# Kernel optimization log

Measured on AMD Instinct MI355X. Metric: run time of the kernel, lower is better.

## Reference

```python
import jax, jax.numpy as jnp
import numpy as np

B, N, L = 256, 4096, 6
EMBED, HID, VOCAB = 16, 32, 200
NOTE, LSTM_D, T = 64, 64, 128


def _tree_structure():
    """One random tree of N nodes (root=node 0), tiled across the batch.
    height = distance above deepest descendant; children have strictly smaller height."""
    rng = np.random.default_rng(0)
    height = np.zeros(N, np.int32)
    height[0] = L
    height[1:] = rng.integers(0, L, N - 1)
    kind = np.full(N, 2, np.int32)  # 2 = internal
    leaf_mask = height == 0
    kind[leaf_mask] = (rng.random(leaf_mask.sum()) < 0.1).astype(np.int32)  # 1=ptr, 0=leaf
    parent = np.zeros(N, np.int64)
    for hl in range(L):
        mask = height == hl
        cand = np.where((height > hl) & (kind == 2))[0]  # root always qualifies
        parent[mask] = rng.choice(cand, size=int(mask.sum()))
    parent[0] = 0  # root points to itself; harmless (its own h stays 0 until final level)
    return height, kind, parent


def setup_inputs():
    height, kind, parent = _tree_structure()
    offs = (np.arange(B, dtype=np.int64) * N)[:, None]
    rng = np.random.default_rng(1)
    inp = {
        'kind': jnp.asarray(np.tile(kind, B), jnp.int32),
        'height': jnp.asarray(np.tile(height, B), jnp.int32),
        'parent': jnp.asarray((parent[None, :] + offs).reshape(-1), jnp.int32),
        'tok_a': jnp.asarray(rng.integers(0, VOCAB, B * N), jnp.int32),
        'tok_b': jnp.asarray(rng.integers(0, VOCAB, B * N), jnp.int32),
        'ptr_time': jnp.asarray(rng.integers(0, T, B * N), jnp.int32),
    }
    key = jax.random.key(0)
    ks = jax.random.split(key, 16)
    def w(k, shape, scale=0.05):
        return (jax.random.normal(k, shape, jnp.float32) * scale)
    inp['first_notes'] = w(ks[0], (B, NOTE), 1.0)
    inp['lstm_out'] = w(ks[1], (B, T, LSTM_D), 1.0)
    inp['embedding'] = w(ks[2], (VOCAB, EMBED), 0.02)
    inp['leaf_w1'] = w(ks[3], (2 * EMBED, HID)); inp['leaf_b1'] = w(ks[4], (HID,))
    inp['leaf_w2'] = w(ks[5], (HID, HID));       inp['leaf_b2'] = w(ks[6], (HID,))
    inp['node_w'] = w(ks[7], (2 * EMBED + HID, HID)); inp['node_b'] = w(ks[8], (HID,))
    inp['ptr_w'] = w(ks[9], (NOTE + LSTM_D, HID));    inp['ptr_b'] = w(ks[10], (HID,))
    inp['ff_w1'] = w(ks[11], (HID, HID)); inp['ff_b1'] = w(ks[12], (HID,))
    inp['ff_w2'] = w(ks[13], (HID, HID)); inp['ff_b2'] = w(ks[14], (HID,))
    inp['tail_w'] = w(ks[15], (HID, 1)); inp['tail_b'] = jnp.zeros((1,), jnp.float32)
    return inp


def reference(kind, height, parent, tok_a, tok_b, ptr_time, first_notes, lstm_out,
              embedding, leaf_w1, leaf_b1, leaf_w2, leaf_b2, node_w, node_b,
              ptr_w, ptr_b, ff_w1, ff_b1, ff_w2, ff_b2, tail_w, tail_b):
    M = kind.shape[0]
    nb = first_notes.shape[0]
    n_per = M // nb
    tree_id = jnp.arange(M, dtype=jnp.int32) // n_per
    emb_a = embedding[tok_a]  # [M, EMBED] (parent-type / first-token embed)
    emb_b = embedding[tok_b]  # [M, EMBED] (node-type / second-token embed)
    pair = jnp.concatenate([emb_a, emb_b], axis=-1)  # [M, 2*EMBED]
    # leaf path: two stacked linears (no nonlinearity), as in leaf_ff
    leaf_h = (pair @ leaf_w1 + leaf_b1) @ leaf_w2 + leaf_b2
    # ptr path: Linear(note_dim + lstm_out_dim -> hidden)
    ptr_in = jnp.concatenate([first_notes[tree_id], lstm_out[tree_id, ptr_time]], axis=-1)
    ptr_h = ptr_in @ ptr_w + ptr_b
    h = jnp.where((kind == 0)[:, None], leaf_h,
                  jnp.where((kind == 1)[:, None], ptr_h, 0.0))
    # level-synchronous child-sum: children always have smaller height
    for lvl in range(1, L + 1):
        csum = jax.ops.segment_sum(h, parent, num_segments=M)  # [M, HID]
        inner = jax.nn.relu(jnp.concatenate([pair, csum], axis=-1) @ node_w + node_b)
        h = jnp.where((height == lvl)[:, None], inner, h)
    roots = h[::n_per]  # [B, HID], root is node 0 of each tree block
    ff = (roots @ ff_w1 + ff_b1) @ ff_w2 + ff_b2
    return ff @ tail_w + tail_b  # [B, 1]


if __name__ == '__main__':
    out = reference(**setup_inputs())
    print(out.shape, out.dtype)
```

## Files before the change

### kernel.cpp

```cpp
#include <hip/hip_runtime.h>

#define BATCH   256
#define N_PER   4096
#define EMBED   16
#define HID     32
#define NOTE    64
#define LSTM_D  64
#define T_LEN   128
#define VOCAB   200
#define HSTR    (BATCH * HID)

#define MH_C0    0
#define MH_C1    1
#define MH_CNT   2
#define MH_P     7
#define MH_PBASE 8
#define OFF_K0N   64
#define OFF_K0S   (OFF_K0N + N_PER)
#define OFF_K1N   (OFF_K0S + N_PER)
#define OFF_K1S   (OFF_K1N + N_PER)
#define OFF_PLIST (OFF_K1S + N_PER)
#define OFF_WSLOT (OFF_PLIST + N_PER)
#define OFF_COFF  (OFF_WSLOT + N_PER)
#define EAW_OFF     (1024 * 1024)
#define EBW_OFF     (EAW_OFF + VOCAB * HID * 4)
#define LA2_OFF     (EBW_OFF + VOCAB * HID * 4)
#define LB2_OFF     (LA2_OFF + VOCAB * HID * 4)
#define CC_OFF      (LB2_OFF + VOCAB * HID * 4)
#define H_OFF       (8ull * 1024 * 1024)

__device__ __forceinline__ unsigned long long shflup64(unsigned long long x, int off) {
    unsigned lo = (unsigned)(x & 0xffffffffull);
    unsigned hi = (unsigned)(x >> 32);
    lo = __shfl_up(lo, off, 64);
    hi = __shfl_up(hi, off, 64);
    return ((unsigned long long)hi << 32) | (unsigned long long)lo;
}

__global__ __launch_bounds__(1024) void build_structure(
    const int* __restrict__ kind, const int* __restrict__ height,
    const int* __restrict__ parent, int* __restrict__ meta,
    const float* __restrict__ embedding,
    const float* __restrict__ leaf_w1, const float* __restrict__ leaf_b1,
    const float* __restrict__ leaf_w2, const float* __restrict__ leaf_b2,
    const float* __restrict__ node_w,
    float* __restrict__ eaw_g, float* __restrict__ ebw_g,
    float* __restrict__ la2, float* __restrict__ lb2, float* __restrict__ cc)
{
    __shared__ unsigned long long wlo[16], whi[16];
    __shared__ int wint[16];
    __shared__ int node2pidx[N_PER];
    __shared__ int deg[N_PER];
    __shared__ int sbases[8];
    __shared__ int stot[8];

    int t  = threadIdx.x;
    int i0 = 4 * t;
    int laneid = t & 63;
    int wid    = t >> 6;

    int par[4], hgt4[4], kn4[4];
    #pragma unroll
    for (int q = 0; q < 4; ++q) {
        par[q]  = parent[i0 + q];
        hgt4[q] = height[i0 + q];
        kn4[q]  = kind[i0 + q];
    }

    int myb[4];
    #pragma unroll
    for (int q = 0; q < 4; ++q) {
        int hgt = hgt4[q];
        int b;
        if (hgt > 0) { b = 1 + hgt; if (b > 7) b = 7; }
        else b = (kn4[q] == 0) ? 0 : 1;
        myb[q] = b;
    }
    unsigned long long clo = 0, chi = 0;
    #pragma unroll
    for (int q = 0; q < 4; ++q) {
        int b = myb[q];
        if (b < 4) clo += 1ull << (16 * b);
        else       chi += 1ull << (16 * (b - 4));
    }

    unsigned long long a = clo, b64 = chi;
    #pragma unroll
    for (int off = 1; off < 64; off <<= 1) {
        unsigned long long ua = shflup64(a, off);
        unsigned long long ub = shflup64(b64, off);
        if (laneid >= off) { a += ua; b64 += ub; }
    }
    if (laneid == 63) { wlo[wid] = a; whi[wid] = b64; }
    __syncthreads();
    unsigned long long blo = 0, bhi = 0;
    for (int w = 0; w < wid; ++w) { blo += wlo[w]; bhi += whi[w]; }
    unsigned long long inc_lo = a + blo, inc_hi = b64 + bhi;
    if (t == 0) {
        unsigned long long tlo = 0, thi = 0;
        for (int w = 0; w < 16; ++w) { tlo += wlo[w]; thi += whi[w]; }
        stot[0] = (int)(tlo & 0xFFFF);         stot[1] = (int)((tlo >> 16) & 0xFFFF);
        stot[2] = (int)((tlo >> 32) & 0xFFFF); stot[3] = (int)((tlo >> 48) & 0xFFFF);
        stot[4] = (int)(thi & 0xFFFF);         stot[5] = (int)((thi >> 16) & 0xFFFF);
        stot[6] = (int)((thi >> 32) & 0xFFFF); stot[7] = (int)((thi >> 48) & 0xFFFF);
        int s = 0;
        for (int bb = 0; bb < 8; ++bb) { sbases[bb] = s; s += stot[bb]; }
        meta[MH_C0] = stot[0];
        meta[MH_C1] = stot[1];
        for (int l = 0; l < 5; ++l) meta[MH_CNT + l]   = stot[2 + l];
        for (int l = 0; l < 5; ++l) meta[MH_PBASE + l] = sbases[2 + l] - sbases[2];
        meta[MH_P] = (sbases[7] - sbases[2]) + stot[7];
    }
    __syncthreads();

    unsigned long long exlo = inc_lo - clo, exhi = inc_hi - chi;
    int mypos[4], mypidx[4];
    #pragma unroll
    for (int q = 0; q < 4; ++q) {
        int i = i0 + q, b = myb[q];
        int pos;
        if (b < 4) { pos = (int)((exlo >> (16 * b)) & 0xFFFF); exlo += 1ull << (16 * b); }
        else       { pos = (int)((exhi >> (16 * (b - 4))) & 0xFFFF); exhi += 1ull << (16 * (b - 4)); }
        mypos[q] = pos;
        int pidx = -1;
        if (b == 0)      meta[OFF_K0N + pos] = i;
        else if (b == 1) meta[OFF_K1N + pos] = i;
        else {
            pidx = (sbases[b] - sbases[2]) + pos;
            meta[OFF_PLIST + pidx] = i;
            node2pidx[i] = pidx;
        }
        mypidx[q] = pidx;
    }
    #pragma unroll
    for (int q = 0; q < 4; ++q) deg[i0 + q] = 0;
    __syncthreads();

    #pragma unroll
    for (int q = 0; q < 4; ++q) {
        int i = i0 + q;
        if (i != 0) atomicAdd(&deg[node2pidx[par[q]]], 1);
    }
    __syncthreads();

    int d0 = deg[i0], d1 = deg[i0 + 1], d2 = deg[i0 + 2], d3 = deg[i0 + 3];
    int s4 = d0 + d1 + d2 + d3;

    int vi = s4;
    #pragma unroll
    for (int off = 1; off < 64; off <<= 1) {
        int u = __shfl_up(vi, off, 64);
        if (laneid >= off) vi += u;
    }
    if (laneid == 63) wint[wid] = vi;
    __syncthreads();
    int bint = 0;
    for (int w = 0; w < wid; ++w) bint += wint[w];
    int incl = vi + bint;

    int ex = incl - s4;
    int o0 = ex, o1 = ex + d0, o2 = o1 + d1, o3 = o2 + d2;
    deg[i0] = o0; deg[i0 + 1] = o1; deg[i0 + 2] = o2; deg[i0 + 3] = o3;
    meta[OFF_COFF + i0]     = o0;
    meta[OFF_COFF + i0 + 1] = o1;
    meta[OFF_COFF + i0 + 2] = o2;
    meta[OFF_COFF + i0 + 3] = o3;
    if (t == 1023) meta[OFF_COFF + N_PER] = o3 + d3;
    __syncthreads();

    #pragma unroll
    for (int q = 0; q < 4; ++q) {
        int i = i0 + q; if (i == 0) continue;
        int slot = atomicAdd(&deg[node2pidx[par[q]]], 1);
        int b = myb[q];
        if (b == 0)      meta[OFF_K0S + mypos[q]] = slot;
        else if (b == 1) meta[OFF_K1S + mypos[q]] = slot;
        else             meta[OFF_WSLOT + mypidx[q]] = slot;
    }

    {
        int hw = t >> 5, ln = t & 31;
        for (int v = hw; v < VOCAB; v += 32) {
            const float* ev = embedding + v * EMBED;
            float ea = 0.f, eb = 0.f, t1a = 0.f, t1b = 0.f;
            #pragma unroll
            for (int k = 0; k < EMBED; ++k) {
                float e = ev[k];
                ea  += e * node_w[k * HID + ln];
                eb  += e * node_w[(EMBED + k) * HID + ln];
                t1a += e * leaf_w1[k * HID + ln];
                t1b += e * leaf_w1[(EMBED + k) * HID + ln];
            }
            eaw_g[v * HID + ln] = ea;
            ebw_g[v * HID + ln] = eb;
            float a2 = 0.f, b2v = 0.f;
            #pragma unroll
            for (int k = 0; k < HID; ++k) {
                float w2 = leaf_w2[k * HID + ln];
                a2  += __shfl(t1a, k, 32) * w2;
                b2v += __shfl(t1b, k, 32) * w2;
            }
            la2[v * HID + ln] = a2;
            lb2[v * HID + ln] = b2v;
        }
        if (t < HID) {
            float c = leaf_b2[t];
            #pragma unroll
            for (int k = 0; k < HID; ++k) c += leaf_b1[k] * leaf_w2[k * HID + t];
            cc[t] = c;
        }
    }
}

__global__ __launch_bounds__(256) void leaf_kernel(
    const int* __restrict__ meta,
    const int* __restrict__ tok_a, const int* __restrict__ tok_b,
    const float* __restrict__ la2, const float* __restrict__ lb2,
    const float* __restrict__ cc,
    float* __restrict__ h)
{
    int lane = threadIdx.x & 31;
    int gid  = (blockIdx.x * blockDim.x + threadIdx.x) >> 5;
    int ngr  = (gridDim.x * blockDim.x) >> 5;

    float ccv = cc[lane];
    int c0 = meta[MH_C0];
    const int* K0N = meta + OFF_K0N;
    const int* K0S = meta + OFF_K0S;
    int tot = c0 * BATCH;

    for (int base = gid * 8; base < tot; base += ngr * 8) {
        int j = base >> 8, tree0 = base & 255;
        int nd = K0N[j], slot = K0S[j];
        int gnb = tree0 * N_PER + nd;
        int ta[8], tb[8];
        #pragma unroll
        for (int q = 0; q < 8; ++q) {
            ta[q] = tok_a[gnb + q * N_PER];
            tb[q] = tok_b[gnb + q * N_PER];
        }
        float* ob = h + (size_t)slot * HSTR + (size_t)tree0 * HID + lane;
        #pragma unroll
        for (int q = 0; q < 8; ++q)
            ob[q * HID] = ccv + la2[ta[q] * HID + lane] + lb2[tb[q] * HID + lane];
    }
}

__global__ __launch_bounds__(256) void ptr_kernel(
    const int* __restrict__ meta, const int* __restrict__ ptr_time,
    const float* __restrict__ first_notes, const float* __restrict__ lstm_out,
    const float* __restrict__ ptr_w, const float* __restrict__ ptr_b,
    float* __restrict__ h)
{
    __shared__ float pw[(NOTE + LSTM_D) * HID];
    for (int x = threadIdx.x; x < (NOTE + LSTM_D) * HID; x += 256)
        pw[x] = ptr_w[x];
    __syncthreads();

    int lane = threadIdx.x & 31;
    int gid  = (blockIdx.x * blockDim.x + threadIdx.x) >> 5;
    int ngr  = (gridDim.x * blockDim.x) >> 5;

    float pb = ptr_b[lane];
    int c1 = meta[MH_C1];
    const int* K1N = meta + OFF_K1N;
    const int* K1S = meta + OFF_K1S;
    int tot = c1 * BATCH;

    for (int i = gid; i < tot; i += ngr) {
        int j = i >> 8, tree = i & 255;
        int node = K1N[j], slot = K1S[j];
        int gn = tree * N_PER + node;
        int tt = ptr_time[gn];
        const float* fn = first_notes + (size_t)tree * NOTE;
        const float* lo = lstm_out + ((size_t)tree * T_LEN + tt) * LSTM_D;
        float v = pb;
        #pragma unroll
        for (int k = 0; k < NOTE; ++k)   v += fn[k] * pw[k * HID + lane];
        #pragma unroll
        for (int k = 0; k < LSTM_D; ++k) v += lo[k] * pw[(NOTE + k) * HID + lane];
        h[(size_t)slot * HSTR + tree * HID + lane] = v;
    }
}

__global__ __launch_bounds__(256) void level_kernel(
    const int* __restrict__ meta,
    const int* __restrict__ tok_a, const int* __restrict__ tok_b,
    const float* __restrict__ eaw_g, const float* __restrict__ ebw_g,
    const float* __restrict__ node_w, const float* __restrict__ node_b,
    float* __restrict__ h, int lvl)
{
    __shared__ float wlds[HID * HID];
    for (int x = threadIdx.x; x < HID * HID; x += 256)
        wlds[x] = node_w[2 * EMBED * HID + x];
    __syncthreads();

    int cnt = meta[MH_CNT + lvl];
    if (cnt == 0) return;
    int pb  = meta[MH_PBASE + lvl];
    const int* PL = meta + OFF_PLIST;
    const int* WS = meta + OFF_WSLOT;
    const int* CO = meta + OFF_COFF;

    int lane = threadIdx.x & 31;
    int gid  = (blockIdx.x * blockDim.x + threadIdx.x) >> 5;
    int ngr  = (gridDim.x * blockDim.x) >> 5;

    float nb = node_b[lane];
    int perchunk = cnt << 5;
    int tot = cnt * BATCH;

    for (int base = gid * 8; base < tot; base += ngr * 8) {
        int tchunk = base / perchunk;
        int r      = base - tchunk * perchunk;
        int tree0  = (tchunk << 5) + (r & 31);
        int pidx   = pb + (r >> 5);

        int node = PL[pidx], wslot = WS[pidx];
        int e0 = CO[pidx], e1 = CO[pidx + 1];

        int gnb = tree0 * N_PER + node;
        int ta[8], tb[8];
        #pragma unroll
        for (int q = 0; q < 8; ++q) {
            ta[q] = tok_a[gnb + q * N_PER];
            tb[q] = tok_b[gnb + q * N_PER];
        }

        float cs[8] = {0.f,0.f,0.f,0.f,0.f,0.f,0.f,0.f};
        const float* hb = h + (size_t)tree0 * HID + lane;
        for (int c = e0; c < e1; ++c) {
            const float* p = hb + (size_t)c * HSTR;
            #pragma unroll
            for (int q = 0; q < 8; ++q) cs[q] += p[q * HID];
        }

        float v[8];
        #pragma unroll
        for (int q = 0; q < 8; ++q)
            v[q] = nb + eaw_g[ta[q] * HID + lane] + ebw_g[tb[q] * HID + lane];

        #pragma unroll
        for (int k = 0; k < HID; ++k) {
            float w = wlds[k * HID + lane];
            #pragma unroll
            for (int q = 0; q < 8; ++q)
                v[q] += __shfl(cs[q], k, 32) * w;
        }

        float* ob = h + (size_t)wslot * HSTR + (size_t)tree0 * HID + lane;
        #pragma unroll
        for (int q = 0; q < 8; ++q)
            ob[q * HID] = fmaxf(v[q], 0.f);
    }
}

__global__ __launch_bounds__(512) void root_final_kernel(
    const int* __restrict__ meta,
    const int* __restrict__ tok_a, const int* __restrict__ tok_b,
    const float* __restrict__ eaw_g, const float* __restrict__ ebw_g,
    const float* __restrict__ h,
    const float* __restrict__ node_w, const float* __restrict__ node_b,
    const float* __restrict__ ff_w1, const float* __restrict__ ff_b1,
    const float* __restrict__ ff_w2, const float* __restrict__ ff_b2,
    const float* __restrict__ tail_w, const float* __restrict__ tail_b,
    float* __restrict__ out)
{
    __shared__ float part[16][33];
    int tree = blockIdx.x;
    int lane = threadIdx.x & 31;
    int g    = threadIdx.x >> 5;

    const int* CO = meta + OFF_COFF;
    int P = meta[MH_P];
    int e = CO[P - 1], e1 = CO[P];

    const float* hb = h + (size_t)tree * HID + lane;
    float s = 0.f;
    for (int c = e + g; c < e1; c += 16)
        s += hb[(size_t)c * HSTR];
    part[g][lane] = s;
    __syncthreads();

    if (g == 0) {
        float csum = part[0][lane];
        #pragma unroll
        for (int k = 1; k < 16; ++k) csum += part[k][lane];

        int gn = tree * N_PER;
        int ta = tok_a[gn], tb = tok_b[gn];
        float v = node_b[lane] + eaw_g[ta * HID + lane] + ebw_g[tb * HID + lane];
        #pragma unroll
        for (int k = 0; k < HID; ++k)
            v += __shfl(csum, k, 32) * node_w[(2 * EMBED + k) * HID + lane];
        v = fmaxf(v, 0.f);

        float f1 = ff_b1[lane];
        #pragma unroll
        for (int k = 0; k < HID; ++k) f1 += __shfl(v, k, 32) * ff_w1[k * HID + lane];
        float f2 = ff_b2[lane];
        #pragma unroll
        for (int k = 0; k < HID; ++k) f2 += __shfl(f1, k, 32) * ff_w2[k * HID + lane];

        float c2 = f2 * tail_w[lane];
        #pragma unroll
        for (int off = 16; off > 0; off >>= 1) c2 += __shfl_down(c2, off, 32);
        if (lane == 0) out[tree] = c2 + tail_b[0];
    }
}

extern "C" void kernel_launch(void* const* d_in, const int* in_sizes, int n_in,
                              void* d_out, int out_size, void* d_ws, size_t ws_size,
                              hipStream_t stream) {
    const int*   kind        = (const int*)d_in[0];
    const int*   height      = (const int*)d_in[1];
    const int*   parent      = (const int*)d_in[2];
    const int*   tok_a       = (const int*)d_in[3];
    const int*   tok_b       = (const int*)d_in[4];
    const int*   ptr_time    = (const int*)d_in[5];
    const float* first_notes = (const float*)d_in[6];
    const float* lstm_out    = (const float*)d_in[7];
    const float* embedding   = (const float*)d_in[8];
    const float* leaf_w1     = (const float*)d_in[9];
    const float* leaf_b1     = (const float*)d_in[10];
    const float* leaf_w2     = (const float*)d_in[11];
    const float* leaf_b2     = (const float*)d_in[12];
    const float* node_w      = (const float*)d_in[13];
    const float* node_b      = (const float*)d_in[14];
    const float* ptr_w       = (const float*)d_in[15];
    const float* ptr_b       = (const float*)d_in[16];
    const float* ff_w1       = (const float*)d_in[17];
    const float* ff_b1       = (const float*)d_in[18];
    const float* ff_w2       = (const float*)d_in[19];
    const float* ff_b2       = (const float*)d_in[20];
    const float* tail_w      = (const float*)d_in[21];
    const float* tail_b      = (const float*)d_in[22];

    char* ws = (char*)d_ws;
    int*   meta    = (int*)ws;
    float* eaw_g   = (float*)(ws + EAW_OFF);
    float* ebw_g   = (float*)(ws + EBW_OFF);
    float* la2     = (float*)(ws + LA2_OFF);
    float* lb2     = (float*)(ws + LB2_OFF);
    float* cc      = (float*)(ws + CC_OFF);
    float* h       = (float*)(ws + H_OFF);

    build_structure<<<1, 1024, 0, stream>>>(
        kind, height, parent, meta,
        embedding, leaf_w1, leaf_b1, leaf_w2, leaf_b2, node_w,
        eaw_g, ebw_g, la2, lb2, cc);

    leaf_kernel<<<2048, 256, 0, stream>>>(
        meta, tok_a, tok_b, la2, lb2, cc, h);

    ptr_kernel<<<1024, 256, 0, stream>>>(
        meta, ptr_time, first_notes, lstm_out, ptr_w, ptr_b, h);

    for (int lvl = 0; lvl < 5; ++lvl) {
        level_kernel<<<1024, 256, 0, stream>>>(
            meta, tok_a, tok_b, eaw_g, ebw_g, node_w, node_b, h, lvl);
    }

    root_final_kernel<<<BATCH, 512, 0, stream>>>(
        meta, tok_a, tok_b, eaw_g, ebw_g, h, node_w, node_b,
        ff_w1, ff_b1, ff_w2, ff_b2, tail_w, tail_b, (float*)d_out);
}
```

Measured before the change: 407.8 us.

## Fuse leaf, ptr, level and root kernels into one per-tree persistent kernel

Replaces the leaf, pointer, five per-level, and root/final kernels with a single kernel that has one 1024-thread block per tree. Levels are separated by block-level __syncthreads instead of kernel launches. This removes eight launches and the device-wide barriers between them, and keeps ptr_w, node_w and first_notes in LDS per block. In exchange, parallelism drops to 256 blocks, the 8-tree batching per wavefront for coalescing and ILP is lost, and each wavefront now handles one tree, so h accesses become strided.

```diff
diff --git a/kernel.cpp b/kernel.cpp
--- a/kernel.cpp
+++ b/kernel.cpp
@@ -212,200 +212,136 @@
     }
 }
 
-__global__ __launch_bounds__(256) void leaf_kernel(
+__global__ __launch_bounds__(1024) void tree_kernel(
     const int* __restrict__ meta,
     const int* __restrict__ tok_a, const int* __restrict__ tok_b,
+    const int* __restrict__ ptr_time,
+    const float* __restrict__ first_notes, const float* __restrict__ lstm_out,
     const float* __restrict__ la2, const float* __restrict__ lb2,
     const float* __restrict__ cc,
-    float* __restrict__ h)
-{
-    int lane = threadIdx.x & 31;
-    int gid  = (blockIdx.x * blockDim.x + threadIdx.x) >> 5;
-    int ngr  = (gridDim.x * blockDim.x) >> 5;
-
-    float ccv = cc[lane];
-    int c0 = meta[MH_C0];
-    const int* K0N = meta + OFF_K0N;
-    const int* K0S = meta + OFF_K0S;
-    int tot = c0 * BATCH;
-
-    for (int base = gid * 8; base < tot; base += ngr * 8) {
-        int j = base >> 8, tree0 = base & 255;
-        int nd = K0N[j], slot = K0S[j];
-        int gnb = tree0 * N_PER + nd;
-        int ta[8], tb[8];
-        #pragma unroll
-        for (int q = 0; q < 8; ++q) {
-            ta[q] = tok_a[gnb + q * N_PER];
-            tb[q] = tok_b[gnb + q * N_PER];
-        }
-        float* ob = h + (size_t)slot * HSTR + (size_t)tree0 * HID + lane;
-        #pragma unroll
-        for (int q = 0; q < 8; ++q)
-            ob[q * HID] = ccv + la2[ta[q] * HID + lane] + lb2[tb[q] * HID + lane];
-    }
-}
-
-__global__ __launch_bounds__(256) void ptr_kernel(
-    const int* __restrict__ meta, const int* __restrict__ ptr_time,
-    const float* __restrict__ first_notes, const float* __restrict__ lstm_out,
     const float* __restrict__ ptr_w, const float* __restrict__ ptr_b,
-    float* __restrict__ h)
-{
-    __shared__ float pw[(NOTE + LSTM_D) * HID];
-    for (int x = threadIdx.x; x < (NOTE + LSTM_D) * HID; x += 256)
-        pw[x] = ptr_w[x];
-    __syncthreads();
-
-    int lane = threadIdx.x & 31;
-    int gid  = (blockIdx.x * blockDim.x + threadIdx.x) >> 5;
-    int ngr  = (gridDim.x * blockDim.x) >> 5;
-
-    float pb = ptr_b[lane];
-    int c1 = meta[MH_C1];
-    const int* K1N = meta + OFF_K1N;
-    const int* K1S = meta + OFF_K1S;
-    int tot = c1 * BATCH;
-
-    for (int i = gid; i < tot; i += ngr) {
-        int j = i >> 8, tree = i & 255;
-        int node = K1N[j], slot = K1S[j];
-        int gn = tree * N_PER + node;
-        int tt = ptr_time[gn];
-        const float* fn = first_notes + (size_t)tree * NOTE;
-        const float* lo = lstm_out + ((size_t)tree * T_LEN + tt) * LSTM_D;
-        float v = pb;
-        #pragma unroll
-        for (int k = 0; k < NOTE; ++k)   v += fn[k] * pw[k * HID + lane];
-        #pragma unroll
-        for (int k = 0; k < LSTM_D; ++k) v += lo[k] * pw[(NOTE + k) * HID + lane];
-        h[(size_t)slot * HSTR + tree * HID + lane] = v;
-    }
-}
-
-__global__ __launch_bounds__(256) void level_kernel(
-    const int* __restrict__ meta,
-    const int* __restrict__ tok_a, const int* __restrict__ tok_b,
     const float* __restrict__ eaw_g, const float* __restrict__ ebw_g,
-    const float* __restrict__ node_w, const float* __restrict__ node_b,
-    float* __restrict__ h, int lvl)
-{
-    __shared__ float wlds[HID * HID];
-    for (int x = threadIdx.x; x < HID * HID; x += 256)
-        wlds[x] = node_w[2 * EMBED * HID + x];
-    __syncthreads();
-
-    int cnt = meta[MH_CNT + lvl];
-    if (cnt == 0) return;
-    int pb  = meta[MH_PBASE + lvl];
-    const int* PL = meta + OFF_PLIST;
-    const int* WS = meta + OFF_WSLOT;
-    const int* CO = meta + OFF_COFF;
-
-    int lane = threadIdx.x & 31;
-    int gid  = (blockIdx.x * blockDim.x + threadIdx.x) >> 5;
-    int ngr  = (gridDim.x * blockDim.x) >> 5;
-
-    float nb = node_b[lane];
-    int perchunk = cnt << 5;
-    int tot = cnt * BATCH;
-
-    for (int base = gid * 8; base < tot; base += ngr * 8) {
-        int tchunk = base / perchunk;
-        int r      = base - tchunk * perchunk;
-        int tree0  = (tchunk << 5) + (r & 31);
-        int pidx   = pb + (r >> 5);
-
-        int node = PL[pidx], wslot = WS[pidx];
-        int e0 = CO[pidx], e1 = CO[pidx + 1];
-
-        int gnb = tree0 * N_PER + node;
-        int ta[8], tb[8];
-        #pragma unroll
-        for (int q = 0; q < 8; ++q) {
-            ta[q] = tok_a[gnb + q * N_PER];
-            tb[q] = tok_b[gnb + q * N_PER];
-        }
-
-        float cs[8] = {0.f,0.f,0.f,0.f,0.f,0.f,0.f,0.f};
-        const float* hb = h + (size_t)tree0 * HID + lane;
-        for (int c = e0; c < e1; ++c) {
-            const float* p = hb + (size_t)c * HSTR;
-            #pragma unroll
-            for (int q = 0; q < 8; ++q) cs[q] += p[q * HID];
-        }
-
-        float v[8];
-        #pragma unroll
-        for (int q = 0; q < 8; ++q)
-            v[q] = nb + eaw_g[ta[q] * HID + lane] + ebw_g[tb[q] * HID + lane];
-
-        #pragma unroll
-        for (int k = 0; k < HID; ++k) {
-            float w = wlds[k * HID + lane];
-            #pragma unroll
-            for (int q = 0; q < 8; ++q)
-                v[q] += __shfl(cs[q], k, 32) * w;
-        }
-
-        float* ob = h + (size_t)wslot * HSTR + (size_t)tree0 * HID + lane;
-        #pragma unroll
-        for (int q = 0; q < 8; ++q)
-            ob[q * HID] = fmaxf(v[q], 0.f);
-    }
-}
-
-__global__ __launch_bounds__(512) void root_final_kernel(
-    const int* __restrict__ meta,
-    const int* __restrict__ tok_a, const int* __restrict__ tok_b,
-    const float* __restrict__ eaw_g, const float* __restrict__ ebw_g,
-    const float* __restrict__ h,
     const float* __restrict__ node_w, const float* __restrict__ node_b,
     const float* __restrict__ ff_w1, const float* __restrict__ ff_b1,
     const float* __restrict__ ff_w2, const float* __restrict__ ff_b2,
     const float* __restrict__ tail_w, const float* __restrict__ tail_b,
-    float* __restrict__ out)
+    float* __restrict__ h, float* __restrict__ out)
 {
+    __shared__ float pw[(NOTE + LSTM_D) * HID];
+    __shared__ float wlds[HID * HID];
+    __shared__ float fnl[NOTE];
     __shared__ float part[16][33];
+
+    int t    = threadIdx.x;
+    int lane = t & 31;
+    int g    = t >> 5;
     int tree = blockIdx.x;
-    int lane = threadIdx.x & 31;
-    int g    = threadIdx.x >> 5;
-
-    const int* CO = meta + OFF_COFF;
-    int P = meta[MH_P];
-    int e = CO[P - 1], e1 = CO[P];
-
-    const float* hb = h + (size_t)tree * HID + lane;
-    float s = 0.f;
-    for (int c = e + g; c < e1; c += 16)
-        s += hb[(size_t)c * HSTR];
-    part[g][lane] = s;
-    __syncthreads();
-
-    if (g == 0) {
-        float csum = part[0][lane];
-        #pragma unroll
-        for (int k = 1; k < 16; ++k) csum += part[k][lane];
-
-        int gn = tree * N_PER;
-        int ta = tok_a[gn], tb = tok_b[gn];
-        float v = node_b[lane] + eaw_g[ta * HID + lane] + ebw_g[tb * HID + lane];
-        #pragma unroll
-        for (int k = 0; k < HID; ++k)
-            v += __shfl(csum, k, 32) * node_w[(2 * EMBED + k) * HID + lane];
-        v = fmaxf(v, 0.f);
-
-        float f1 = ff_b1[lane];
-        #pragma unroll
-        for (int k = 0; k < HID; ++k) f1 += __shfl(v, k, 32) * ff_w1[k * HID + lane];
-        float f2 = ff_b2[lane];
-        #pragma unroll
-        for (int k = 0; k < HID; ++k) f2 += __shfl(f1, k, 32) * ff_w2[k * HID + lane];
-
-        float c2 = f2 * tail_w[lane];
-        #pragma unroll
-        for (int off = 16; off > 0; off >>= 1) c2 += __shfl_down(c2, off, 32);
-        if (lane == 0) out[tree] = c2 + tail_b[0];
+
+    for (int x = t; x < (NOTE + LSTM_D) * HID; x += 1024) pw[x] = ptr_w[x];
+    for (int x = t; x < HID * HID; x += 1024) wlds[x] = node_w[2 * EMBED * HID + x];
+    if (t < NOTE) fnl[t] = first_notes[(size_t)tree * NOTE + t];
+    __syncthreads();
+
+    const int* K0N = meta + OFF_K0N;
+    const int* K0S = meta + OFF_K0S;
+    const int* K1N = meta + OFF_K1N;
+    const int* K1S = meta + OFF_K1S;
+    const int* PL  = meta + OFF_PLIST;
+    const int* WS  = meta + OFF_WSLOT;
+    const int* CO  = meta + OFF_COFF;
+
+    {
+        float ccv = cc[lane];
+        int c0 = meta[MH_C0];
+        for (int j = g; j < c0; j += 32) {
+            int nd = K0N[j], slot = K0S[j];
+            int gn = tree * N_PER + nd;
+            int ta = tok_a[gn], tb = tok_b[gn];
+            h[(size_t)slot * HSTR + tree * HID + lane] =
+                ccv + la2[ta * HID + lane] + lb2[tb * HID + lane];
+        }
+    }
+
+    {
+        float pb = ptr_b[lane];
+        int c1 = meta[MH_C1];
+        for (int j = g; j < c1; j += 32) {
+            int nd = K1N[j], slot = K1S[j];
+            int gn = tree * N_PER + nd;
+            int tt = ptr_time[gn];
+            const float* lo = lstm_out + ((size_t)tree * T_LEN + tt) * LSTM_D;
+            float v = pb;
+            #pragma unroll
+            for (int k = 0; k < NOTE; ++k)   v += fnl[k] * pw[k * HID + lane];
+            #pragma unroll
+            for (int k = 0; k < LSTM_D; ++k) v += lo[k] * pw[(NOTE + k) * HID + lane];
+            h[(size_t)slot * HSTR + tree * HID + lane] = v;
+        }
+    }
+    __syncthreads();
+
+    float nb = node_b[lane];
+    for (int lvl = 0; lvl < 5; ++lvl) {
+        int cnt   = meta[MH_CNT + lvl];
+        int pbase = meta[MH_PBASE + lvl];
+        for (int pp = g; pp < cnt; pp += 32) {
+            int pidx = pbase + pp;
+            int node = PL[pidx], wslot = WS[pidx];
+            int e0 = CO[pidx], e1 = CO[pidx + 1];
+
+            int gn = tree * N_PER + node;
+            int ta = tok_a[gn], tb = tok_b[gn];
+
+            float csum = 0.f;
+            const float* hb = h + (size_t)tree * HID + lane;
+            for (int c = e0; c < e1; ++c) csum += hb[(size_t)c * HSTR];
+
+            float v = nb + eaw_g[ta * HID + lane] + ebw_g[tb * HID + lane];
+            #pragma unroll
+            for (int k = 0; k < HID; ++k)
+                v += __shfl(csum, k, 32) * wlds[k * HID + lane];
+            h[(size_t)wslot * HSTR + tree * HID + lane] = fmaxf(v, 0.f);
+        }
+        __syncthreads();
+    }
+
+    {
+        int P = meta[MH_P];
+        int e = CO[P - 1], e1 = CO[P];
+        const float* hb = h + (size_t)tree * HID + lane;
+        if (g < 16) {
+            float s = 0.f;
+            for (int c = e + g; c < e1; c += 16)
+                s += hb[(size_t)c * HSTR];
+            part[g][lane] = s;
+        }
+        __syncthreads();
+
+        if (g == 0) {
+            float csum = part[0][lane];
+            #pragma unroll
+            for (int k = 1; k < 16; ++k) csum += part[k][lane];
+
+            int gn = tree * N_PER;
+            int ta = tok_a[gn], tb = tok_b[gn];
+            float v = nb + eaw_g[ta * HID + lane] + ebw_g[tb * HID + lane];
+            #pragma unroll
+            for (int k = 0; k < HID; ++k)
+                v += __shfl(csum, k, 32) * wlds[k * HID + lane];
+            v = fmaxf(v, 0.f);
+
+            float f1 = ff_b1[lane];
+            #pragma unroll
+            for (int k = 0; k < HID; ++k) f1 += __shfl(v, k, 32) * ff_w1[k * HID + lane];
+            float f2 = ff_b2[lane];
+            #pragma unroll
+            for (int k = 0; k < HID; ++k) f2 += __shfl(f1, k, 32) * ff_w2[k * HID + lane];
+
+            float c2 = f2 * tail_w[lane];
+            #pragma unroll
+            for (int off = 16; off > 0; off >>= 1) c2 += __shfl_down(c2, off, 32);
+            if (lane == 0) out[tree] = c2 + tail_b[0];
+        }
     }
 }
 
@@ -450,18 +386,9 @@
         embedding, leaf_w1, leaf_b1, leaf_w2, leaf_b2, node_w,
         eaw_g, ebw_g, la2, lb2, cc);
 
-    leaf_kernel<<<2048, 256, 0, stream>>>(
-        meta, tok_a, tok_b, la2, lb2, cc, h);
-
-    ptr_kernel<<<1024, 256, 0, stream>>>(
-        meta, ptr_time, first_notes, lstm_out, ptr_w, ptr_b, h);
-
-    for (int lvl = 0; lvl < 5; ++lvl) {
-        level_kernel<<<1024, 256, 0, stream>>>(
-            meta, tok_a, tok_b, eaw_g, ebw_g, node_w, node_b, h, lvl);
-    }
-
-    root_final_kernel<<<BATCH, 512, 0, stream>>>(
-        meta, tok_a, tok_b, eaw_g, ebw_g, h, node_w, node_b,
-        ff_w1, ff_b1, ff_w2, ff_b2, tail_w, tail_b, (float*)d_out);
+    tree_kernel<<<BATCH, 1024, 0, stream>>>(
+        meta, tok_a, tok_b, ptr_time, first_notes, lstm_out,
+        la2, lb2, cc, ptr_w, ptr_b, eaw_g, ebw_g, node_w, node_b,
+        ff_w1, ff_b1, ff_w2, ff_b2, tail_w, tail_b,
+        h, (float*)d_out);
 }
```

New measurement: 404.4 us. Within noise of the previous version (-0.8%).
